# Optimization experiments

Measured on AMD Instinct MI355X. Metric: run time of the kernel, lower is better.

## Reference

```python
import jax, jax.numpy as jnp
import numpy as np

HEAD_NUM = 16
NEG_BIG = -2.0**32 + 1.0


def _pos_encoding(T, D):
    pos = np.arange(T)[:, None].astype(np.float64)
    i = np.arange(D)[None, :].astype(np.float64)
    angle = pos / np.power(10000.0, 2.0 * i / D)
    pe = np.empty((T, D), dtype=np.float64)
    pe[:, 0::2] = np.sin(angle[:, 0::2])
    pe[:, 1::2] = np.cos(angle[:, 1::2])
    return jnp.asarray(pe * (D ** 0.5), dtype=jnp.float32)  # scale=True


def setup_inputs() -> dict:
    key = jax.random.key(0)
    ks = jax.random.split(key, 9)
    B, T, D = 32, 512, 1024
    return {
        "queries": jax.random.normal(ks[0], (B, T, D), jnp.float32),
        "keys": jax.random.normal(ks[1], (B, T, D), jnp.float32),
        "query_masks": jax.random.randint(ks[2], (B, 1), 1, T + 1, jnp.int32),
        "key_masks": jax.random.randint(ks[3], (B, 1), 1, T + 1, jnp.int32),
        "W_Query": jax.random.normal(ks[4], (D, D), jnp.float32) * 0.02,
        "W_key": jax.random.normal(ks[5], (D, D), jnp.float32) * 0.02,
        "W_Value": jax.random.normal(ks[6], (D, D), jnp.float32) * 0.02,
        "fw1": jax.random.normal(ks[7], (D, 4 * D), jnp.float32) * 0.02,
        "fw2": jax.random.normal(ks[8], (4 * D, D), jnp.float32) * 0.02,
    }


def reference(queries, keys, query_masks, key_masks, W_Query, W_key, W_Value, fw1, fw2):
    B, T, D = queries.shape
    h = HEAD_NUM
    d = D // h
    pe = _pos_encoding(T, D)  # [T, D]

    # faithful to source: queries get PE; keys = PE(queries_with_PE) (keys input unused)
    q_pe = queries + pe[None]
    k_pe = q_pe + pe[None]

    qs = jnp.einsum('btd,de->bte', q_pe, W_Query)
    ks_ = jnp.einsum('btd,de->bte', k_pe, W_key)
    vs = jnp.einsum('btd,de->bte', ks_, W_Value)  # faithful: values from projected keys

    def split_heads(x):  # [B,T,h*d] -> [h,B,T,d] (matches tf.split/concat on axis 0)
        return x.reshape(B, T, h, d).transpose(2, 0, 1, 3)

    q4, k4, v4 = split_heads(qs), split_heads(ks_), split_heads(vs)

    scores = jnp.einsum('hbqd,hbkd->hbqk', q4, k4) / (d ** 0.5)

    pos = jnp.arange(T)
    km = (pos[None, :] < key_masks).astype(jnp.float32)    # [B,T]
    qm = (pos[None, :] < query_masks).astype(jnp.float32)  # [B,T]

    scores = jnp.where(km[None, :, None, :] == 1.0, scores, NEG_BIG)
    scores = scores - jnp.max(scores, axis=-1, keepdims=True)
    attn = jax.nn.softmax(scores, axis=-1)
    attn = attn * qm[None, :, :, None]

    out = jnp.einsum('hbqk,hbkd->hbqd', attn, v4)
    result = out.transpose(1, 2, 0, 3).reshape(B, T, D)  # merge heads (head-major)

    result = result + q_pe  # use_res
    # feed forward (use_layer_norm=False, no dropout at inference)
    hmid = jax.nn.relu(jnp.einsum('btd,df->btf', result, fw1))
    result = result + jnp.einsum('btf,fd->btd', hmid, fw2)

    # output_type == 'mean'
    return jnp.mean(result, axis=1, keepdims=True)  # [B,1,D]
```

## Files before the change

### kernel.cpp

```cpp
#include <hip/hip_runtime.h>

constexpr int B_  = 32;
constexpr int T_  = 512;
constexpr int D_  = 1024;
constexpr int NH_ = 16;
constexpr int DH_ = 64;
constexpr int F_  = 4096;
constexpr int BT_ = B_ * T_;

typedef __attribute__((ext_vector_type(8))) short bf16x8;
typedef __attribute__((ext_vector_type(4))) float f32x4;
typedef __attribute__((ext_vector_type(8))) int i32x8;

#define DEVI __device__ __forceinline__

DEVI unsigned short f2bf(float f) {
  union { float f; unsigned u; } uf; uf.f = f;
  unsigned r = uf.u + 0x7fffu + ((uf.u >> 16) & 1u);
  return (unsigned short)(r >> 16);
}
DEVI float b2f(unsigned short h) {
  union { unsigned u; float f; } uf; uf.u = ((unsigned)h) << 16;
  return uf.f;
}
DEVI unsigned char f2fp8(float f) {
  return (unsigned char)(__builtin_amdgcn_cvt_pk_fp8_f32(f, f, 0, false) & 0xFF);
}
DEVI long kperm(long c) {
  long blk = c & ~127L; int k7 = (int)(c & 127);
  return blk | (((k7 >> 4) & 1) << 6) | ((k7 >> 5) << 4) | (k7 & 15);
}
DEVI void gload16(const void* g, void* l) {
  __builtin_amdgcn_global_load_lds(
      (const __attribute__((address_space(1))) void*)(uintptr_t)g,
      (__attribute__((address_space(3))) void*)(unsigned)(uintptr_t)l, 16, 0, 0);
}
DEVI i32x8 ld32(const char* p0, const char* p1) {
  int4 lo = *(const int4*)p0, hi = *(const int4*)p1;
  i32x8 r;
  r[0] = lo.x; r[1] = lo.y; r[2] = lo.z; r[3] = lo.w;
  r[4] = hi.x; r[5] = hi.y; r[6] = hi.z; r[7] = hi.w;
  return r;
}

__global__ void pack_kernel(const float* __restrict__ q,
                            unsigned short* __restrict__ q_pe, unsigned short* __restrict__ k_pe) {
  long i = ((long)blockIdx.x * 256 + threadIdx.x) * 4;
  const float4 qv = *(const float4*)(q + i);
  int t = (int)((i >> 10) & 511);
  int j0 = (int)(i & 1023);
  float pvv[4];
#pragma unroll
  for (int u = 0; u < 4; u++) {
    int j = j0 + u;
    float inv = exp2f(-(2.0f * (float)j / 1024.0f) * 13.2877123795494f);
    float ang = (float)t * inv;
    pvv[u] = ((j & 1) ? cosf(ang) : sinf(ang)) * 32.0f;
  }
  ushort4 a, b;
  a.x = f2bf(qv.x + pvv[0]); a.y = f2bf(qv.y + pvv[1]);
  a.z = f2bf(qv.z + pvv[2]); a.w = f2bf(qv.w + pvv[3]);
  b.x = f2bf(qv.x + 2.f * pvv[0]); b.y = f2bf(qv.y + 2.f * pvv[1]);
  b.z = f2bf(qv.z + 2.f * pvv[2]); b.w = f2bf(qv.w + 2.f * pvv[3]);
  *(ushort4*)(q_pe + i) = a;
  *(ushort4*)(k_pe + i) = b;
}

__global__ void prep_w(const float* __restrict__ Wq, const float* __restrict__ Wk,
                       const float* __restrict__ Wv, const float* __restrict__ fw1,
                       unsigned short* __restrict__ Wqt, unsigned short* __restrict__ Wkt,
                       unsigned short* __restrict__ Wvt, unsigned char* __restrict__ fw1t8,
                       unsigned short* __restrict__ Wkbf) {
  const int z = blockIdx.z;
  if (z < 3 && blockIdx.x >= 32) return;
  const float* W = (z == 0) ? Wq : (z == 1) ? Wk : (z == 2) ? Wv : fw1;
  unsigned short* Wt = (z == 0) ? Wqt : (z == 1) ? Wkt : Wvt;
  const int N = (z == 3) ? F_ : D_;
  __shared__ float tile[32][33];
  int tx = threadIdx.x & 31, ty = threadIdx.x >> 5;
  int bx = blockIdx.x, by = blockIdx.y;
  for (int i = 0; i < 4; i++) {
    int r = by * 32 + ty + i * 8;
    float v = W[(long)r * N + bx * 32 + tx];
    tile[ty + i * 8][tx] = v;
    if (z == 1) Wkbf[(long)r * D_ + bx * 32 + tx] = f2bf(v);
  }
  __syncthreads();
  for (int i = 0; i < 4; i++) {
    int r = bx * 32 + ty + i * 8;
    if (z == 3) fw1t8[(long)r * D_ + kperm(by * 32 + tx)] = f2fp8(tile[tx][ty + i * 8] * 64.0f);
    else        Wt[(long)r * D_ + by * 32 + tx] = f2bf(tile[tx][ty + i * 8]);
  }
}

template <int EPI>
__global__ __launch_bounds__(256) void gemm_bt(
    const unsigned short* __restrict__ A0, const unsigned short* __restrict__ Bt0,
    unsigned short* __restrict__ C0, float* __restrict__ hacc, int M, int N, int K) {
  __shared__ unsigned short As[128 * 32];
  __shared__ unsigned short Bs[128 * 32];
  const unsigned short* A  = A0;
  const unsigned short* Bt = Bt0;
  unsigned short* C        = C0;

  const int tid = threadIdx.x;
  const int lane = tid & 63, w = tid >> 6;
  const int wr = w >> 1, wc = w & 1;
  const int l15 = lane & 15, lhi = lane >> 4;
  const int brow = blockIdx.y * 128, bcol = blockIdx.x * 128;

  f32x4 acc[4][4] = {};
  const int o = tid * 16;
  const int srow = o >> 6;
  const int skel = (o & 63) >> 1;

  for (int kk = 0; kk < K; kk += 32) {
    gload16(A + (long)(brow + srow) * K + kk + skel,        (char*)As + o);
    gload16(A + (long)(brow + srow + 64) * K + kk + skel,   (char*)As + o + 4096);
    gload16(Bt + (long)(bcol + srow) * K + kk + skel,       (char*)Bs + o);
    gload16(Bt + (long)(bcol + srow + 64) * K + kk + skel,  (char*)Bs + o + 4096);
    __syncthreads();
    bf16x8 af[4], bfr[4];
    for (int m = 0; m < 4; m++)
      af[m] = *(const bf16x8*)((const char*)As + ((wr * 64 + m * 16 + l15) * 64 + lhi * 16));
    for (int n = 0; n < 4; n++)
      bfr[n] = *(const bf16x8*)((const char*)Bs + ((wc * 64 + n * 16 + l15) * 64 + lhi * 16));
    for (int m = 0; m < 4; m++)
      for (int n = 0; n < 4; n++)
        acc[m][n] = __builtin_amdgcn_mfma_f32_16x16x32_bf16(af[m], bfr[n], acc[m][n], 0, 0, 0);
    __syncthreads();
  }

  for (int m = 0; m < 4; m++)
    for (int n = 0; n < 4; n++) {
      int row = brow + wr * 64 + m * 16 + lhi * 4;
      int col = bcol + wc * 64 + n * 16 + l15;
      for (int r = 0; r < 4; r++)
        C[(long)(row + r) * N + col] = f2bf(acc[m][n][r]);
    }
}

template <int EPI>
__global__ __launch_bounds__(512, 2) void gemm8(
    const unsigned short* __restrict__ A0, const unsigned short* __restrict__ Bt0, unsigned short* __restrict__ C0,
    const unsigned short* __restrict__ A1, const unsigned short* __restrict__ Bt1, unsigned short* __restrict__ C1,
    const unsigned short* __restrict__ A2, const unsigned short* __restrict__ Bt2, unsigned short* __restrict__ C2,
    float* __restrict__ hacc, int N,
    const int* __restrict__ L0, const int* __restrict__ L1, const int* __restrict__ L2) {
  constexpr int K = 1024, NK = 16, NI = 8;
  __shared__ char lds[2][2][32768];

  const int z = blockIdx.z;
  const unsigned short* A  = (z == 0) ? A0  : (z == 1 ? A1  : A2);
  const unsigned short* Bt = (z == 0) ? Bt0 : (z == 1 ? Bt1 : Bt2);
  unsigned short* C        = (z == 0) ? C0  : (z == 1 ? C1  : C2);
  const int* L             = (z == 0) ? L0  : (z == 1 ? L1  : L2);

  const long brow = (long)blockIdx.x * 256, bcol = (long)blockIdx.y * 256;
  if (L && (brow & 256) && L[brow >> 9] <= 256) return;

  const int tid = threadIdx.x;
  const int lane = tid & 63, w = tid >> 6;
  const int wm = w >> 2, wn = w & 3;
  const int l15 = lane & 15, lhi = lane >> 4;

  const int drow = (tid * 16) >> 7;
  const int dcol = ((tid * 16) & 127) ^ ((drow & 7) << 4);
  const int sw   = (l15 & 7) << 4;

  f32x4 acc[8][4] = {};
  bf16x8 bfr[4][2], af[2][2];

  auto STAGE = [&](const unsigned short* __restrict__ P, long tb, int kt, int h, int buf, int op) {
    const unsigned short* g = P + (tb + h * 128 + drow) * (long)K + kt * 64 + (dcol >> 1);
    char* l = &lds[buf][op][h * 16384 + tid * 16];
    gload16(g, l);
    gload16(g + 64L * K, l + 8192);
  };
  auto LDA = [&](int buf, int q) {
#pragma unroll
    for (int mi = 0; mi < 2; mi++) {
      int row = wm * 128 + (q * 2 + mi) * 16 + l15;
#pragma unroll
      for (int kk = 0; kk < 2; kk++)
        af[mi][kk] = *(const bf16x8*)(&lds[buf][0][0] + (row << 7) + ((kk * 64 + lhi * 16) ^ sw));
    }
  };
  auto LDB = [&](int buf) {
#pragma unroll
    for (int n = 0; n < 4; n++) {
      int row = wn * 64 + n * 16 + l15;
#pragma unroll
      for (int kk = 0; kk < 2; kk++)
        bfr[n][kk] = *(const bf16x8*)(&lds[buf][1][0] + (row << 7) + ((kk * 64 + lhi * 16) ^ sw));
    }
  };
  auto MFMAQ = [&](int q) {
    __builtin_amdgcn_s_setprio(1);
#pragma unroll
    for (int mi = 0; mi < 2; mi++)
#pragma unroll
      for (int n = 0; n < 4; n++)
#pragma unroll
        for (int kk = 0; kk < 2; kk++)
          acc[q * 2 + mi][n] =
              __builtin_amdgcn_mfma_f32_16x16x32_bf16(af[mi][kk], bfr[n][kk], acc[q * 2 + mi][n], 0, 0, 0);
    __builtin_amdgcn_s_setprio(0);
  };
#define BAR() __builtin_amdgcn_s_barrier()
#define GATE4() asm volatile("s_waitcnt vmcnt(4)" ::: "memory")

  STAGE(A, brow, 0, 0, 0, 0);  STAGE(A, brow, 0, 1, 0, 0);
  STAGE(Bt, bcol, 0, 0, 0, 1); STAGE(Bt, bcol, 0, 1, 0, 1);
  STAGE(Bt, bcol, 1, 0, 1, 1); STAGE(Bt, bcol, 1, 1, 1, 1);
  GATE4();
  BAR();

  for (int i = 0; i < NI; ++i) {
    const int k1 = 2 * i + 1;
    const int ka = (2 * i + 2) & (NK - 1);
    const int kb = (2 * i + 3) & (NK - 1);
    LDA(0, 0); LDB(0); STAGE(A, brow, k1, 0, 1, 0);
    BAR(); MFMAQ(0); BAR();
    LDA(0, 1);         STAGE(A, brow, k1, 1, 1, 0);
    BAR(); MFMAQ(1); BAR();
    LDA(0, 2);         STAGE(Bt, bcol, ka, 0, 0, 1);
    BAR(); MFMAQ(2); BAR();
    LDA(0, 3);         STAGE(Bt, bcol, ka, 1, 0, 1);
    BAR(); MFMAQ(3);
    GATE4();
    BAR();
    LDA(1, 0); LDB(1); STAGE(A, brow, ka, 0, 0, 0);
    BAR(); MFMAQ(0); BAR();
    LDA(1, 1);         STAGE(A, brow, ka, 1, 0, 0);
    BAR(); MFMAQ(1); BAR();
    LDA(1, 2);         STAGE(Bt, bcol, kb, 0, 1, 1);
    BAR(); MFMAQ(2); BAR();
    LDA(1, 3);         STAGE(Bt, bcol, kb, 1, 1, 1);
    BAR(); MFMAQ(3);
    GATE4();
    BAR();
  }
#undef BAR
#undef GATE4

  if (EPI == 0) {
    if (z == 2) {
      asm volatile("s_waitcnt vmcnt(0)" ::: "memory");
      __builtin_amdgcn_s_barrier();
      char* tl = &lds[0][0][0] + (w << 14);
#pragma unroll
      for (int m = 0; m < 8; m++)
#pragma unroll
        for (int n = 0; n < 4; n++) {
          int cl = n * 16 + l15;
#pragma unroll
          for (int r = 0; r < 4; r++) {
            int tofs = m * 16 + lhi * 4 + r;
            *(unsigned short*)(tl + cl * 256 + ((tofs * 2) ^ ((cl & 7) << 4))) = f2bf(acc[m][n][r]);
          }
        }
      asm volatile("" ::: "memory");
      const int bb = (int)(brow >> 9), t0 = (int)(brow & 511);
#pragma unroll
      for (int rr = 0; rr < 16; rr++) {
        int row = rr * 4 + lhi;
        bf16x8 v = *(const bf16x8*)(tl + row * 256 + ((l15 * 16) ^ ((row & 7) << 4)));
        int gcol = (int)bcol + wn * 64 + row;
        long vtrow = ((long)(bb * NH_ + (gcol >> 6))) * DH_ + (gcol & 63);
        *(bf16x8*)(C + vtrow * T_ + t0 + wm * 128 + l15 * 8) = v;
      }
    } else {
#pragma unroll
      for (int m = 0; m < 8; m++)
#pragma unroll
        for (int n = 0; n < 4; n++) {
          long row = brow + wm * 128 + m * 16 + lhi * 4;
          long col = bcol + wn * 64 + n * 16 + l15;
#pragma unroll
          for (int r = 0; r < 4; r++)
            C[(row + r) * (long)N + col] = f2bf(acc[m][n][r]);
        }
    }
  } else {
    const int batch = (int)(brow >> 9);
#pragma unroll
    for (int n = 0; n < 4; n++) {
      float t = 0.f;
#pragma unroll
      for (int m = 0; m < 8; m++)
#pragma unroll
        for (int r = 0; r < 4; r++) t += fmaxf(acc[m][n][r], 0.f);
      t += __shfl_xor(t, 16);
      t += __shfl_xor(t, 32);
      if (lane < 16)
        atomicAdd(hacc + (long)batch * F_ + bcol + wn * 64 + n * 16 + l15, t);
    }
  }
}

__global__ __launch_bounds__(512, 2) void gemmf8(
    const unsigned char* __restrict__ A, const unsigned char* __restrict__ Bt,
    float* __restrict__ hacc) {
  constexpr int K = 1024, NKT = 8, NI = 4;
  __shared__ char lds[2][2][32768];
  const long brow = (long)blockIdx.x * 256, bcol = (long)blockIdx.y * 256;
  const int tid = threadIdx.x;
  const int lane = tid & 63, w = tid >> 6;
  const int wm = w >> 2, wn = w & 3;
  const int l15 = lane & 15, lhi = lane >> 4;

  const int drow = (tid * 16) >> 7;
  const int dcol = ((tid * 16) & 127) ^ ((drow & 7) << 4);
  const int sw   = (l15 & 7) << 4;

  f32x4 acc[8][4] = {};
  i32x8 af[2], bfr[4];

  auto STAGE = [&](const unsigned char* __restrict__ P, long tb, int kt, int h, int buf, int op) {
    const unsigned char* g = P + (tb + h * 128 + drow) * (long)K + kt * 128 + dcol;
    char* l = &lds[buf][op][h * 16384 + tid * 16];
    gload16(g, l);
    gload16(g + 64L * K, l + 8192);
  };
  auto LDA = [&](int buf, int q) {
#pragma unroll
    for (int mi = 0; mi < 2; mi++) {
      int row = wm * 128 + (q * 2 + mi) * 16 + l15;
      const char* base = &lds[buf][0][0] + (row << 7);
      af[mi] = ld32(base + ((lhi * 16) ^ sw), base + ((64 + lhi * 16) ^ sw));
    }
  };
  auto LDB = [&](int buf) {
#pragma unroll
    for (int n = 0; n < 4; n++) {
      int row = wn * 64 + n * 16 + l15;
      const char* base = &lds[buf][1][0] + (row << 7);
      bfr[n] = ld32(base + ((lhi * 16) ^ sw), base + ((64 + lhi * 16) ^ sw));
    }
  };
  auto MFMAQ = [&](int q) {
    __builtin_amdgcn_s_setprio(1);
#pragma unroll
    for (int mi = 0; mi < 2; mi++)
#pragma unroll
      for (int n = 0; n < 4; n++)
        acc[q * 2 + mi][n] = __builtin_amdgcn_mfma_scale_f32_16x16x128_f8f6f4(
            af[mi], bfr[n], acc[q * 2 + mi][n], 0, 0,
            0, 0x7F7F7F7F, 0, 0x7F7F7F7F);
    __builtin_amdgcn_s_setprio(0);
  };
#define BAR() __builtin_amdgcn_s_barrier()
#define GATE4() asm volatile("s_waitcnt vmcnt(4)" ::: "memory")

  STAGE(A, brow, 0, 0, 0, 0);  STAGE(A, brow, 0, 1, 0, 0);
  STAGE(Bt, bcol, 0, 0, 0, 1); STAGE(Bt, bcol, 0, 1, 0, 1);
  STAGE(Bt, bcol, 1, 0, 1, 1); STAGE(Bt, bcol, 1, 1, 1, 1);
  GATE4();
  BAR();

  for (int i = 0; i < NI; ++i) {
    const int k1 = 2 * i + 1;
    const int ka = (2 * i + 2) & (NKT - 1);
    const int kb = (2 * i + 3) & (NKT - 1);
    LDA(0, 0); LDB(0); STAGE(A, brow, k1, 0, 1, 0);
    BAR(); MFMAQ(0); BAR();
    LDA(0, 1);         STAGE(A, brow, k1, 1, 1, 0);
    BAR(); MFMAQ(1); BAR();
    LDA(0, 2);         STAGE(Bt, bcol, ka, 0, 0, 1);
    BAR(); MFMAQ(2); BAR();
    LDA(0, 3);         STAGE(Bt, bcol, ka, 1, 0, 1);
    BAR(); MFMAQ(3);
    GATE4();
    BAR();
    LDA(1, 0); LDB(1); STAGE(A, brow, ka, 0, 0, 0);
    BAR(); MFMAQ(0); BAR();
    LDA(1, 1);         STAGE(A, brow, ka, 1, 0, 0);
    BAR(); MFMAQ(1); BAR();
    LDA(1, 2);         STAGE(Bt, bcol, kb, 0, 1, 1);
    BAR(); MFMAQ(2); BAR();
    LDA(1, 3);         STAGE(Bt, bcol, kb, 1, 1, 1);
    BAR(); MFMAQ(3);
    GATE4();
    BAR();
  }
#undef BAR
#undef GATE4

  const int batch = (int)(brow >> 9);
#pragma unroll
  for (int n = 0; n < 4; n++) {
    float t = 0.f;
#pragma unroll
    for (int m = 0; m < 8; m++)
#pragma unroll
      for (int r = 0; r < 4; r++) t += fmaxf(acc[m][n][r], 0.f);
    t += __shfl_xor(t, 16);
    t += __shfl_xor(t, 32);
    if (lane < 16)
      atomicAdd(hacc + (long)batch * F_ + bcol + wn * 64 + n * 16 + l15, t);
  }
}

__global__ __launch_bounds__(256, 3) void attn_kernel(
    const unsigned short* __restrict__ qs, const unsigned short* __restrict__ ks,
    const unsigned short* __restrict__ vt, const unsigned short* __restrict__ q_pe,
    const int* __restrict__ qmask, const int* __restrict__ kmask,
    unsigned char* __restrict__ res8, float* __restrict__ racc) {
  __shared__ unsigned short Ks[2][64 * 64];
  __shared__ unsigned short Vs[2][64 * 64];
  __shared__ unsigned short Ps[4][32 * 64];

  const int tid = threadIdx.x, lane = tid & 63, w = tid >> 6;
  const int l15 = lane & 15, lhi = lane >> 4;
  const int h = blockIdx.x, b = blockIdx.y, q0 = blockIdx.z * 128;
  const int qlen = qmask[b], kvlen = kmask[b];

  if (q0 >= qlen) {
    int cc = tid & 63;
    float s = 0.f;
    for (int i = 0; i < 32; i++) {
      int r = (tid >> 6) * 32 + i;
      long rb = (long)(b * T_ + q0 + r) * D_;
      long col = h * DH_ + cc;
      float v = b2f(q_pe[rb + col]);
      res8[rb + kperm(col)] = f2fp8(v);
      s += v;
    }
    atomicAdd(racc + b * D_ + h * DH_ + cc, s);
    return;
  }

  bf16x8 qf[2][2];
  for (int m = 0; m < 2; m++)
    for (int k2 = 0; k2 < 2; k2++) {
      int t = q0 + w * 32 + m * 16 + l15;
      qf[m][k2] = *(const bf16x8*)(qs + (long)(b * T_ + t) * D_ + h * DH_ + k2 * 32 + lhi * 8);
    }

  f32x4 o[2][4] = {};
  float mrun[2][4], lrun[2][4];
  for (int m = 0; m < 2; m++)
    for (int r = 0; r < 4; r++) { mrun[m][r] = -3e38f; lrun[m][r] = 0.f; }

  const float SCL = 0.125f * 1.4426950408889634f;
  const float THR = 8.0f / SCL;
  const int nc = (kvlen + 63) >> 6;

  auto stage = [&](int c, int buf) {
#pragma unroll
    for (int cl = 0; cl < 2; cl++) {
      int ob = cl * 4096 + tid * 16;
      int os = ob ^ (((ob >> 7) & 7) << 4);
      int r0 = os >> 7, cb = os & 127;
      gload16(ks + (long)(b * T_ + c * 64 + r0) * D_ + h * DH_ + (cb >> 1),
              (char*)&Ks[buf][0] + ob);
      gload16(vt + ((long)(b * NH_ + h) * DH_ + r0) * T_ + c * 64 + (cb >> 1),
              (char*)&Vs[buf][0] + ob);
    }
  };

  stage(0, 0);
  int cur = 0;
  for (int c = 0; c < nc; c++) {
    const int nxt = (c + 1 < nc) ? c + 1 : c;
    stage(nxt, cur ^ 1);
    asm volatile("s_waitcnt vmcnt(4)" ::: "memory");
    __builtin_amdgcn_sched_barrier(0);
    __builtin_amdgcn_s_barrier();

    f32x4 s[2][4] = {};
    for (int k2 = 0; k2 < 2; k2++)
      for (int n = 0; n < 4; n++) {
        int key = n * 16 + l15;
        int Ab = key * 128 + (k2 * 32 + lhi * 8) * 2;
        bf16x8 kf = *(const bf16x8*)((const char*)&Ks[cur][0] + (Ab ^ ((key & 7) << 4)));
        s[0][n] = __builtin_amdgcn_mfma_f32_16x16x32_bf16(qf[0][k2], kf, s[0][n], 0, 0, 0);
        s[1][n] = __builtin_amdgcn_mfma_f32_16x16x32_bf16(qf[1][k2], kf, s[1][n], 0, 0, 0);
      }

    if (c == nc - 1) {
      for (int n = 0; n < 4; n++)
        if (c * 64 + n * 16 + l15 >= kvlen)
          for (int m = 0; m < 2; m++) s[m][n] = f32x4{-3e38f, -3e38f, -3e38f, -3e38f};
    }

    for (int m = 0; m < 2; m++) {
      float mx[4];
      for (int r = 0; r < 4; r++) {
        float v = s[m][0][r];
        for (int n = 1; n < 4; n++) v = fmaxf(v, s[m][n][r]);
        mx[r] = v;
      }
      for (int msk = 1; msk < 16; msk <<= 1)
        for (int r = 0; r < 4; r++) mx[r] = fmaxf(mx[r], __shfl_xor(mx[r], msk));
      bool grow = false;
      for (int r = 0; r < 4; r++) grow = grow || (mx[r] > mrun[m][r] + THR);
      if (__any(grow)) {
        float corr[4];
        for (int r = 0; r < 4; r++) {
          float mn = fmaxf(mrun[m][r], mx[r]);
          corr[r] = exp2f((mrun[m][r] - mn) * SCL);
          mrun[m][r] = mn;
        }
        for (int nd = 0; nd < 4; nd++)
          for (int r = 0; r < 4; r++) o[m][nd][r] *= corr[r];
        for (int r = 0; r < 4; r++) lrun[m][r] *= corr[r];
      }
      float ps[4] = {0.f, 0.f, 0.f, 0.f};
      for (int n = 0; n < 4; n++)
        for (int r = 0; r < 4; r++) {
          float pval = exp2f((s[m][n][r] - mrun[m][r]) * SCL);
          s[m][n][r] = pval;
          ps[r] += pval;
        }
      for (int msk = 1; msk < 16; msk <<= 1)
        for (int r = 0; r < 4; r++) ps[r] += __shfl_xor(ps[r], msk);
      for (int r = 0; r < 4; r++) lrun[m][r] += ps[r];
      for (int n = 0; n < 4; n++)
        for (int r = 0; r < 4; r++) {
          int row = m * 16 + lhi * 4 + r;
          int Ab = row * 128 + (n * 16 + l15) * 2;
          *(unsigned short*)((char*)&Ps[w][0] + (Ab ^ ((row & 7) << 4))) = f2bf(s[m][n][r]);
        }
    }
    asm volatile("" ::: "memory");

    for (int k4 = 0; k4 < 2; k4++) {
      bf16x8 pa[2];
      for (int m = 0; m < 2; m++) {
        int row = m * 16 + l15;
        int Ab = row * 128 + k4 * 64 + lhi * 16;
        pa[m] = *(const bf16x8*)((const char*)&Ps[w][0] + (Ab ^ ((row & 7) << 4)));
      }
      for (int nd = 0; nd < 4; nd++) {
        int dv = nd * 16 + l15;
        int Ab = dv * 128 + k4 * 64 + lhi * 16;
        bf16x8 vb = *(const bf16x8*)((const char*)&Vs[cur][0] + (Ab ^ ((dv & 7) << 4)));
        for (int m = 0; m < 2; m++)
          o[m][nd] = __builtin_amdgcn_mfma_f32_16x16x32_bf16(pa[m], vb, o[m][nd], 0, 0, 0);
      }
    }
    __builtin_amdgcn_s_barrier();
    cur ^= 1;
  }

  float cs[4] = {0.f, 0.f, 0.f, 0.f};
  for (int m = 0; m < 2; m++)
    for (int r = 0; r < 4; r++) {
      int t = q0 + w * 32 + m * 16 + lhi * 4 + r;
      float inv = 1.0f / lrun[m][r];
      bool valid = t < qlen;
      long rb = (long)(b * T_ + t) * D_;
      for (int nd = 0; nd < 4; nd++) {
        long col = h * DH_ + nd * 16 + l15;
        float v = valid ? o[m][nd][r] * inv : 0.f;
        float val = v + b2f(q_pe[rb + col]);
        res8[rb + kperm(col)] = f2fp8(val);
        cs[nd] += val;
      }
    }
  for (int nd = 0; nd < 4; nd++) {
    cs[nd] += __shfl_xor(cs[nd], 16);
    cs[nd] += __shfl_xor(cs[nd], 32);
  }
  if (lane < 16)
    for (int nd = 0; nd < 4; nd++)
      atomicAdd(racc + b * D_ + h * DH_ + nd * 16 + l15, cs[nd]);
}

__global__ void final_kernel(const float* __restrict__ hacc, const float* __restrict__ fw2,
                             const float* __restrict__ racc, float* __restrict__ out) {
  int n = blockIdx.x * 64 + (threadIdx.x & 63);
  int bg = threadIdx.x >> 6;
  int f0 = blockIdx.y * 512;
  float acc[8] = {};
  for (int f = f0; f < f0 + 512; f++) {
    float wv = fw2[(long)f * D_ + n];
    for (int i = 0; i < 8; i++) acc[i] += hacc[(long)(bg * 8 + i) * F_ + f] * wv;
  }
  for (int i = 0; i < 8; i++) {
    float v = acc[i] * (1.0f / (512.0f * 64.0f));
    if (blockIdx.y == 0) v += racc[(long)(bg * 8 + i) * D_ + n] * (1.0f / 512.0f);
    atomicAdd(out + (bg * 8 + i) * D_ + n, v);
  }
}

extern "C" void kernel_launch(void* const* d_in, const int* in_sizes, int n_in,
                              void* d_out, int out_size, void* d_ws, size_t ws_size,
                              hipStream_t stream) {
  const float* queries = (const float*)d_in[0];
  const int*   qmask = (const int*)d_in[2];
  const int*   kmask = (const int*)d_in[3];
  const float* Wq  = (const float*)d_in[4];
  const float* Wk  = (const float*)d_in[5];
  const float* Wv  = (const float*)d_in[6];
  const float* fw1 = (const float*)d_in[7];
  const float* fw2 = (const float*)d_in[8];
  float* out = (float*)d_out;

  char* p = (char*)d_ws;
  auto alloc = [&](size_t bytes) -> char* {
    char* r = p; p += (bytes + 255) & ~(size_t)255; return r;
  };
  unsigned short* q_pe = (unsigned short*)alloc((size_t)BT_ * D_ * 2);
  unsigned short* k_pe = (unsigned short*)alloc((size_t)BT_ * D_ * 2);
  unsigned short* qs   = (unsigned short*)alloc((size_t)BT_ * D_ * 2);
  unsigned short* ksb  = (unsigned short*)alloc((size_t)BT_ * D_ * 2);
  unsigned short* vt   = (unsigned short*)alloc((size_t)BT_ * D_ * 2);
  unsigned char*  res8 = (unsigned char*)alloc((size_t)BT_ * D_);
  unsigned short* Wqt  = (unsigned short*)alloc((size_t)D_ * D_ * 2);
  unsigned short* Wkt  = (unsigned short*)alloc((size_t)D_ * D_ * 2);
  unsigned short* Wvt  = (unsigned short*)alloc((size_t)D_ * D_ * 2);
  unsigned short* Wkbf = (unsigned short*)alloc((size_t)D_ * D_ * 2);
  unsigned short* Wkvt = (unsigned short*)alloc((size_t)D_ * D_ * 2);
  unsigned char*  fw1t8 = (unsigned char*)alloc((size_t)D_ * F_);
  float*          racc = (float*)alloc((size_t)B_ * D_ * 4);
  float*          hacc = (float*)alloc((size_t)B_ * F_ * 4);

  hipMemsetAsync(hacc, 0, (size_t)B_ * F_ * 4, stream);
  hipMemsetAsync(racc, 0, (size_t)B_ * D_ * 4, stream);
  hipMemsetAsync(out, 0, (size_t)B_ * D_ * 4, stream);

  pack_kernel<<<BT_ * D_ / 1024, 256, 0, stream>>>(queries, q_pe, k_pe);
  prep_w<<<dim3(128, 32, 4), 256, 0, stream>>>(Wq, Wk, Wv, fw1, Wqt, Wkt, Wvt, fw1t8, Wkbf);

  gemm_bt<0><<<dim3(8, 8, 1), 256, 0, stream>>>(Wvt, Wkbf, Wkvt, nullptr, D_, D_, D_);

  gemm8<0><<<dim3(64, 4, 3), 512, 0, stream>>>(q_pe, Wqt, qs,
                                               k_pe, Wkt, ksb,
                                               k_pe, Wkvt, vt,
                                               nullptr, D_, qmask, kmask, kmask);

  attn_kernel<<<dim3(16, 32, 4), 256, 0, stream>>>(qs, ksb, vt, q_pe, qmask, kmask, res8, racc);

  gemmf8<<<dim3(64, 16), 512, 0, stream>>>(res8, fw1t8, hacc);

  final_kernel<<<dim3(16, 8), 256, 0, stream>>>(hacc, fw2, racc, out);
}
```

Baseline: 379.4 us.

## Drop k_pe buffer by adding precomputed PE projections in GEMM epilogue

Since k_pe = q_pe + pe, the key and value projections are rewritten as q_pe·W plus a per-position pe·W term. That term is precomputed once for 512 positions and added in the gemm8 epilogue, which removes the full k_pe write and its reads. The epilogue now does an extra bf16 gather per output element. fw2 is also cast to bf16 in a separate kernel, so final_kernel reads half the bytes, but the cast itself adds a pass over fw2. The change also adds several small launches and introduces extra rounding.

After: 431.4 us. 1.14x slower.

```diff
diff --git a/kernel.cpp b/kernel.cpp
--- a/kernel.cpp
+++ b/kernel.cpp
@@ -42,28 +42,42 @@
   r[4] = hi.x; r[5] = hi.y; r[6] = hi.z; r[7] = hi.w;
   return r;
 }
-
-__global__ void pack_kernel(const float* __restrict__ q,
-                            unsigned short* __restrict__ q_pe, unsigned short* __restrict__ k_pe) {
+DEVI float pe_val(int t, int j) {
+  float inv = exp2f(-(2.0f * (float)j / 1024.0f) * 13.2877123795494f);
+  float ang = (float)t * inv;
+  return ((j & 1) ? cosf(ang) : sinf(ang)) * 32.0f;
+}
+
+__global__ void pack_kernel(const float* __restrict__ q, unsigned short* __restrict__ q_pe) {
   long i = ((long)blockIdx.x * 256 + threadIdx.x) * 4;
   const float4 qv = *(const float4*)(q + i);
   int t = (int)((i >> 10) & 511);
   int j0 = (int)(i & 1023);
-  float pvv[4];
-#pragma unroll
-  for (int u = 0; u < 4; u++) {
-    int j = j0 + u;
-    float inv = exp2f(-(2.0f * (float)j / 1024.0f) * 13.2877123795494f);
-    float ang = (float)t * inv;
-    pvv[u] = ((j & 1) ? cosf(ang) : sinf(ang)) * 32.0f;
-  }
-  ushort4 a, b;
-  a.x = f2bf(qv.x + pvv[0]); a.y = f2bf(qv.y + pvv[1]);
-  a.z = f2bf(qv.z + pvv[2]); a.w = f2bf(qv.w + pvv[3]);
-  b.x = f2bf(qv.x + 2.f * pvv[0]); b.y = f2bf(qv.y + 2.f * pvv[1]);
-  b.z = f2bf(qv.z + 2.f * pvv[2]); b.w = f2bf(qv.w + 2.f * pvv[3]);
+  ushort4 a;
+  a.x = f2bf(qv.x + pe_val(t, j0));
+  a.y = f2bf(qv.y + pe_val(t, j0 + 1));
+  a.z = f2bf(qv.z + pe_val(t, j0 + 2));
+  a.w = f2bf(qv.w + pe_val(t, j0 + 3));
   *(ushort4*)(q_pe + i) = a;
-  *(ushort4*)(k_pe + i) = b;
+}
+
+__global__ void pe16_kernel(unsigned short* __restrict__ pe16) {
+  int i = (blockIdx.x * 256 + threadIdx.x) * 4;
+  int t = (i >> 10) & 511, j0 = i & 1023;
+  ushort4 o;
+  o.x = f2bf(pe_val(t, j0));
+  o.y = f2bf(pe_val(t, j0 + 1));
+  o.z = f2bf(pe_val(t, j0 + 2));
+  o.w = f2bf(pe_val(t, j0 + 3));
+  *(ushort4*)(pe16 + i) = o;
+}
+
+__global__ void cast_fw2(const float* __restrict__ W, unsigned short* __restrict__ Wb) {
+  long i = ((long)blockIdx.x * 256 + threadIdx.x) * 4;
+  const float4 v = *(const float4*)(W + i);
+  ushort4 o;
+  o.x = f2bf(v.x); o.y = f2bf(v.y); o.z = f2bf(v.z); o.w = f2bf(v.w);
+  *(ushort4*)(Wb + i) = o;
 }
 
 __global__ void prep_w(const float* __restrict__ Wq, const float* __restrict__ Wk,
@@ -146,7 +160,8 @@
     const unsigned short* __restrict__ A1, const unsigned short* __restrict__ Bt1, unsigned short* __restrict__ C1,
     const unsigned short* __restrict__ A2, const unsigned short* __restrict__ Bt2, unsigned short* __restrict__ C2,
     float* __restrict__ hacc, int N,
-    const int* __restrict__ L0, const int* __restrict__ L1, const int* __restrict__ L2) {
+    const int* __restrict__ L0, const int* __restrict__ L1, const int* __restrict__ L2,
+    const unsigned short* __restrict__ PE1, const unsigned short* __restrict__ PE2) {
   constexpr int K = 1024, NK = 16, NI = 8;
   __shared__ char lds[2][2][32768];
 
@@ -155,6 +170,7 @@
   const unsigned short* Bt = (z == 0) ? Bt0 : (z == 1 ? Bt1 : Bt2);
   unsigned short* C        = (z == 0) ? C0  : (z == 1 ? C1  : C2);
   const int* L             = (z == 0) ? L0  : (z == 1 ? L1  : L2);
+  const unsigned short* peadd = (z == 1) ? PE1 : (z == 2 ? PE2 : nullptr);
 
   const long brow = (long)blockIdx.x * 256, bcol = (long)blockIdx.y * 256;
   if (L && (brow & 256) && L[brow >> 9] <= 256) return;
@@ -249,19 +265,22 @@
       asm volatile("s_waitcnt vmcnt(0)" ::: "memory");
       __builtin_amdgcn_s_barrier();
       char* tl = &lds[0][0][0] + (w << 14);
+      const int t0 = (int)(brow & 511);
 #pragma unroll
       for (int m = 0; m < 8; m++)
 #pragma unroll
         for (int n = 0; n < 4; n++) {
           int cl = n * 16 + l15;
+          int gc = (int)bcol + wn * 64 + cl;
 #pragma unroll
           for (int r = 0; r < 4; r++) {
             int tofs = m * 16 + lhi * 4 + r;
-            *(unsigned short*)(tl + cl * 256 + ((tofs * 2) ^ ((cl & 7) << 4))) = f2bf(acc[m][n][r]);
+            float v = acc[m][n][r] + b2f(peadd[(long)(t0 + wm * 128 + tofs) * D_ + gc]);
+            *(unsigned short*)(tl + cl * 256 + ((tofs * 2) ^ ((cl & 7) << 4))) = f2bf(v);
           }
         }
       asm volatile("" ::: "memory");
-      const int bb = (int)(brow >> 9), t0 = (int)(brow & 511);
+      const int bb = (int)(brow >> 9);
 #pragma unroll
       for (int rr = 0; rr < 16; rr++) {
         int row = rr * 4 + lhi;
@@ -278,8 +297,11 @@
           long row = brow + wm * 128 + m * 16 + lhi * 4;
           long col = bcol + wn * 64 + n * 16 + l15;
 #pragma unroll
-          for (int r = 0; r < 4; r++)
-            C[(row + r) * (long)N + col] = f2bf(acc[m][n][r]);
+          for (int r = 0; r < 4; r++) {
+            float v = acc[m][n][r];
+            if (peadd) v += b2f(peadd[(long)((row + r) & 511) * D_ + col]);
+            C[(row + r) * (long)N + col] = f2bf(v);
+          }
         }
     }
   } else {
@@ -569,14 +591,14 @@
       atomicAdd(racc + b * D_ + h * DH_ + nd * 16 + l15, cs[nd]);
 }
 
-__global__ void final_kernel(const float* __restrict__ hacc, const float* __restrict__ fw2,
+__global__ void final_kernel(const float* __restrict__ hacc, const unsigned short* __restrict__ fw2b,
                              const float* __restrict__ racc, float* __restrict__ out) {
   int n = blockIdx.x * 64 + (threadIdx.x & 63);
   int bg = threadIdx.x >> 6;
   int f0 = blockIdx.y * 512;
   float acc[8] = {};
   for (int f = f0; f < f0 + 512; f++) {
-    float wv = fw2[(long)f * D_ + n];
+    float wv = b2f(fw2b[(long)f * D_ + n]);
     for (int i = 0; i < 8; i++) acc[i] += hacc[(long)(bg * 8 + i) * F_ + f] * wv;
   }
   for (int i = 0; i < 8; i++) {
@@ -604,7 +626,6 @@
     char* r = p; p += (bytes + 255) & ~(size_t)255; return r;
   };
   unsigned short* q_pe = (unsigned short*)alloc((size_t)BT_ * D_ * 2);
-  unsigned short* k_pe = (unsigned short*)alloc((size_t)BT_ * D_ * 2);
   unsigned short* qs   = (unsigned short*)alloc((size_t)BT_ * D_ * 2);
   unsigned short* ksb  = (unsigned short*)alloc((size_t)BT_ * D_ * 2);
   unsigned short* vt   = (unsigned short*)alloc((size_t)BT_ * D_ * 2);
@@ -615,6 +636,10 @@
   unsigned short* Wkbf = (unsigned short*)alloc((size_t)D_ * D_ * 2);
   unsigned short* Wkvt = (unsigned short*)alloc((size_t)D_ * D_ * 2);
   unsigned char*  fw1t8 = (unsigned char*)alloc((size_t)D_ * F_);
+  unsigned short* fw2b = (unsigned short*)alloc((size_t)D_ * F_ * 2);
+  unsigned short* pe16 = (unsigned short*)alloc((size_t)T_ * D_ * 2);
+  unsigned short* peWk = (unsigned short*)alloc((size_t)T_ * D_ * 2);
+  unsigned short* peWkv= (unsigned short*)alloc((size_t)T_ * D_ * 2);
   float*          racc = (float*)alloc((size_t)B_ * D_ * 4);
   float*          hacc = (float*)alloc((size_t)B_ * F_ * 4);
 
@@ -622,19 +647,23 @@
   hipMemsetAsync(racc, 0, (size_t)B_ * D_ * 4, stream);
   hipMemsetAsync(out, 0, (size_t)B_ * D_ * 4, stream);
 
-  pack_kernel<<<BT_ * D_ / 1024, 256, 0, stream>>>(queries, q_pe, k_pe);
+  pack_kernel<<<BT_ * D_ / 1024, 256, 0, stream>>>(queries, q_pe);
+  pe16_kernel<<<T_ * D_ / 1024, 256, 0, stream>>>(pe16);
   prep_w<<<dim3(128, 32, 4), 256, 0, stream>>>(Wq, Wk, Wv, fw1, Wqt, Wkt, Wvt, fw1t8, Wkbf);
+  cast_fw2<<<F_ * D_ / 1024, 256, 0, stream>>>(fw2, fw2b);
 
   gemm_bt<0><<<dim3(8, 8, 1), 256, 0, stream>>>(Wvt, Wkbf, Wkvt, nullptr, D_, D_, D_);
+  gemm_bt<0><<<dim3(8, 4, 1), 256, 0, stream>>>(pe16, Wkt, peWk, nullptr, T_, D_, D_);
+  gemm_bt<0><<<dim3(8, 4, 1), 256, 0, stream>>>(pe16, Wkvt, peWkv, nullptr, T_, D_, D_);
 
   gemm8<0><<<dim3(64, 4, 3), 512, 0, stream>>>(q_pe, Wqt, qs,
-                                               k_pe, Wkt, ksb,
-                                               k_pe, Wkvt, vt,
-                                               nullptr, D_, qmask, kmask, kmask);
+                                               q_pe, Wkt, ksb,
+                                               q_pe, Wkvt, vt,
+                                               nullptr, D_, qmask, kmask, kmask, peWk, peWkv);
 
   attn_kernel<<<dim3(16, 32, 4), 256, 0, stream>>>(qs, ksb, vt, q_pe, qmask, kmask, res8, racc);
 
   gemmf8<<<dim3(64, 16), 512, 0, stream>>>(res8, fw1t8, hacc);
 
-  final_kernel<<<dim3(16, 8), 256, 0, stream>>>(hacc, fw2, racc, out);
-}
+  final_kernel<<<dim3(16, 8), 256, 0, stream>>>(hacc, fw2b, racc, out);
+}
```
